# Kernel tuning notes

Hardware: AMD Instinct MI355X
Metric: run time of the kernel (lower is better)

Reference implementation:

```python
import jax, jax.numpy as jnp
import numpy as np

N_NODES = 50000
N_EDGES = 100000
NUM_RELS = 200
IN_DIM = 64
OUT_DIM = 64


def setup_inputs() -> dict:
    key = jax.random.key(0)
    k1, k2, k3, k4, k5, k6 = jax.random.split(key, 6)
    input_h = jax.random.normal(k1, (N_NODES, IN_DIM), dtype=jnp.float32)
    src = jax.random.randint(k2, (N_EDGES,), 0, N_NODES, dtype=jnp.int32)
    rel = jax.random.randint(k3, (N_EDGES,), 0, NUM_RELS, dtype=jnp.int32)
    dst = jax.random.randint(k4, (N_EDGES,), 0, N_NODES, dtype=jnp.int32)
    edges = jnp.stack([src, rel, dst], axis=1)  # (E, 3)
    # xavier_normal for relation weight: std = sqrt(2/(in+out))
    w_std = float(np.sqrt(2.0 / (IN_DIM + OUT_DIM)))
    weight = jax.random.normal(k5, (NUM_RELS, IN_DIM, OUT_DIM), dtype=jnp.float32) * w_std
    # xavier_uniform with leaky_relu(0.2) gain for self-loop weight
    gain = float(np.sqrt(2.0 / (1.0 + 0.2 ** 2)))
    bound = gain * float(np.sqrt(6.0 / (IN_DIM + OUT_DIM)))
    self_loop_weight = jax.random.uniform(
        k6, (IN_DIM, OUT_DIM), dtype=jnp.float32, minval=-bound, maxval=bound)
    return {"input_h": input_h, "edges": edges, "weight": weight,
            "self_loop_weight": self_loop_weight}


def reference(input_h, edges, weight, self_loop_weight):
    src, rel, dst = edges[:, 0], edges[:, 1], edges[:, 2]
    num_nodes = input_h.shape[0]
    num_edges = edges.shape[0]

    src_h = input_h[src]                      # (E, in) gather
    w_e = weight[rel]                         # (E, in, out) per-edge weight materialization
    msg = jnp.einsum('ei,eio->eo', src_h, w_e)  # per-edge bmm

    # torch quirk: index_matrix[dst] = arange(E) keeps the LAST write per dst,
    # so each edge's message is replaced by the message of the last edge
    # (in edge order) with the same destination.
    last_idx = jax.ops.segment_max(jnp.arange(num_edges, dtype=jnp.int32), dst,
                                   num_segments=num_nodes)  # (N,)
    msg = msg[last_idx[dst]]                  # (E, out)

    # scatter-mean aggregation by destination (nodes with no in-edges get 0)
    msg_sum = jax.ops.segment_sum(msg, dst, num_segments=num_nodes)          # (N, out)
    count = jax.ops.segment_sum(jnp.ones((num_edges,), msg.dtype), dst,
                                num_segments=num_nodes)                      # (N,)
    agg = jnp.where(count[:, None] > 0, msg_sum / jnp.maximum(count, 1.0)[:, None], 0.0)

    out = input_h @ self_loop_weight + agg    # self-loop plus aggregated messages
    return out
```

## Files before the change

kernel.cpp:

```cpp
#include <hip/hip_runtime.h>

#define N_NODES 50000
#define N_EDGES 100000
#define NUM_RELS 200
#define DIM 64
#define CAP 512
#define TILES 8
#define KPAD 72

typedef __attribute__((ext_vector_type(8))) short bf16x8;
typedef __attribute__((ext_vector_type(8))) unsigned short u16x8;
typedef __attribute__((ext_vector_type(4))) float f32x4;

#define OFF_LAST 0
#define OFF_CUR  50000
#define OFF_BN   50200
#define OFF_BS   152600
#define HB_OFF   1020032u
#define WT_OFF   7420032u

__device__ __forceinline__ unsigned short f2bf(float x) {
    union { float f; unsigned u; } v; v.f = x;
    unsigned r = v.u + 0x7FFFu + ((v.u >> 16) & 1u);
    return (unsigned short)(r >> 16);
}

#define PREP_INIT 197
#define PREP_WT   201
#define PREP_HB   782

__global__ __launch_bounds__(256) void prep_kernel(
    const float* __restrict__ h, const float* __restrict__ weight,
    const float* __restrict__ wself, int* __restrict__ ws,
    unsigned short* __restrict__ hb, unsigned short* __restrict__ wt)
{
    __shared__ float Wl[DIM * DIM];
    int b = blockIdx.x, t = threadIdx.x;

    if (b < PREP_INIT) {
        int i = b * 256 + t;
        if (i < N_NODES) ws[OFF_LAST + i] = -1;
        if (i < NUM_RELS) ws[OFF_CUR + i] = 0;
        return;
    }
    if (b < PREP_INIT + PREP_WT) {
        int rel = b - PREP_INIT;
        const float* src = (rel < NUM_RELS) ? (weight + (size_t)rel * DIM * DIM) : wself;
#pragma unroll
        for (int j = 0; j < 16; ++j) Wl[t + j * 256] = src[t + j * 256];
        __syncthreads();
        int c = t >> 2, q = t & 3;
        unsigned short tmp[16];
#pragma unroll
        for (int kk = 0; kk < 16; ++kk)
            tmp[kk] = f2bf(Wl[(q * 16 + kk) * DIM + c]);
        unsigned short* dst = wt + (size_t)rel * DIM * DIM + c * DIM + q * 16;
        *(u16x8*)dst       = *(const u16x8*)&tmp[0];
        *(u16x8*)(dst + 8) = *(const u16x8*)&tmp[8];
        return;
    }
    {
        long off = (long)(b - PREP_INIT - PREP_WT) * 4096 + (long)t * 16;
        if (off < (long)N_NODES * DIM) {
            const float4* src = (const float4*)(h + off);
            unsigned short tmp[16];
#pragma unroll
            for (int j = 0; j < 4; ++j) {
                float4 v = src[j];
                tmp[j*4+0]=f2bf(v.x); tmp[j*4+1]=f2bf(v.y);
                tmp[j*4+2]=f2bf(v.z); tmp[j*4+3]=f2bf(v.w);
            }
            *(u16x8*)(hb + off)     = *(const u16x8*)&tmp[0];
            *(u16x8*)(hb + off + 8) = *(const u16x8*)&tmp[8];
        }
    }
}

__global__ void edge_max_kernel(const int* __restrict__ edges, int* __restrict__ ws) {
    int e = blockIdx.x * 256 + threadIdx.x;
    if (e < N_EDGES) atomicMax(&ws[OFF_LAST + edges[e * 3 + 2]], e);
}

#define BUCKET_BLKS 196
#define NODE_TILES 782

__global__ __launch_bounds__(256) void bucket_self_kernel(
    const int* __restrict__ edges, const unsigned short* __restrict__ hb,
    const unsigned short* __restrict__ wt, int* __restrict__ ws,
    float* __restrict__ out)
{
    __shared__ unsigned short Wsh[DIM * KPAD];
    __shared__ unsigned short Hs[DIM * KPAD];
    int t = threadIdx.x;

    if (blockIdx.x < BUCKET_BLKS) {
        int n = blockIdx.x * 256 + t;
        if (n < N_NODES) {
            int li = ws[OFF_LAST + n];
            if (li >= 0) {
                int r = edges[li * 3 + 1];
                int s = edges[li * 3 + 0];
                int pos = atomicAdd(&ws[OFF_CUR + r], 1);
                if (pos < CAP) {
                    ws[OFF_BN + r * CAP + pos] = n;
                    ws[OFF_BS + r * CAP + pos] = s;
                }
            }
        }
        return;
    }

    int base = (blockIdx.x - BUCKET_BLKS) * 64;
    int row = t >> 2, q = t & 3;
    {
        const unsigned short* wsrc = wt + (size_t)NUM_RELS * DIM * DIM + row * DIM + q * 16;
        *(u16x8*)&Wsh[row * KPAD + q * 16]     = *(const u16x8*)wsrc;
        *(u16x8*)&Wsh[row * KPAD + q * 16 + 8] = *(const u16x8*)(wsrc + 8);
        int n = base + row; if (n >= N_NODES) n = N_NODES - 1;
        const unsigned short* hsrc = hb + (size_t)n * DIM + q * 16;
        *(u16x8*)&Hs[row * KPAD + q * 16]     = *(const u16x8*)hsrc;
        *(u16x8*)&Hs[row * KPAD + q * 16 + 8] = *(const u16x8*)(hsrc + 8);
    }
    __syncthreads();

    int l = t & 63;
    int w = __builtin_amdgcn_readfirstlane(t >> 6);
    int r16 = l & 15, kb = l >> 4;

    bf16x8 a0 = *reinterpret_cast<const bf16x8*>(&Hs[(w * 16 + r16) * KPAD + kb * 8]);
    bf16x8 a1 = *reinterpret_cast<const bf16x8*>(&Hs[(w * 16 + r16) * KPAD + 32 + kb * 8]);

    int nn[4]; bool vv[4];
#pragma unroll
    for (int r = 0; r < 4; ++r) {
        nn[r] = base + w * 16 + kb * 4 + r;
        vv[r] = nn[r] < N_NODES;
    }

#pragma unroll
    for (int n4 = 0; n4 < 4; ++n4) {
        bf16x8 b0 = *reinterpret_cast<const bf16x8*>(&Wsh[(n4 * 16 + r16) * KPAD + kb * 8]);
        bf16x8 b1 = *reinterpret_cast<const bf16x8*>(&Wsh[(n4 * 16 + r16) * KPAD + 32 + kb * 8]);
        f32x4 acc = {0.f, 0.f, 0.f, 0.f};
        acc = __builtin_amdgcn_mfma_f32_16x16x32_bf16(a0, b0, acc, 0, 0, 0);
        acc = __builtin_amdgcn_mfma_f32_16x16x32_bf16(a1, b1, acc, 0, 0, 0);
#pragma unroll
        for (int r = 0; r < 4; ++r)
            if (vv[r]) out[(size_t)nn[r] * DIM + n4 * 16 + r16] = acc[r];
    }
}

__global__ __launch_bounds__(256) void msg_kernel(
    const unsigned short* __restrict__ hb, const unsigned short* __restrict__ wt,
    const int* __restrict__ ws, float* __restrict__ out)
{
    __shared__ unsigned short Wsh[DIM * KPAD];
    __shared__ unsigned short Hs[DIM * KPAD];

    int rel = blockIdx.x >> 3;
    int tile = blockIdx.x & 7;
    int c = ws[OFF_CUR + rel];
    if (c > CAP) c = CAP;
    int start = tile * 64;
    if (start >= c) return;

    int t = threadIdx.x;
    const int* bn = ws + OFF_BN + rel * CAP;
    const int* bs = ws + OFF_BS + rel * CAP;

    int row = t >> 2, q = t & 3;
    {
        const unsigned short* wsrc = wt + (size_t)rel * DIM * DIM + row * DIM + q * 16;
        *(u16x8*)&Wsh[row * KPAD + q * 16]     = *(const u16x8*)wsrc;
        *(u16x8*)&Wsh[row * KPAD + q * 16 + 8] = *(const u16x8*)(wsrc + 8);
        int pos = start + row; if (pos >= c) pos = c - 1;
        int s = bs[pos];
        const unsigned short* hsrc = hb + (size_t)s * DIM + q * 16;
        *(u16x8*)&Hs[row * KPAD + q * 16]     = *(const u16x8*)hsrc;
        *(u16x8*)&Hs[row * KPAD + q * 16 + 8] = *(const u16x8*)(hsrc + 8);
    }
    __syncthreads();

    int l = t & 63;
    int w = __builtin_amdgcn_readfirstlane(t >> 6);
    int r16 = l & 15, kb = l >> 4;

    bf16x8 a0 = *reinterpret_cast<const bf16x8*>(&Hs[(w * 16 + r16) * KPAD + kb * 8]);
    bf16x8 a1 = *reinterpret_cast<const bf16x8*>(&Hs[(w * 16 + r16) * KPAD + 32 + kb * 8]);

    int nn[4]; bool vv[4];
#pragma unroll
    for (int r = 0; r < 4; ++r) {
        int p = start + w * 16 + kb * 4 + r;
        vv[r] = p < c;
        nn[r] = bn[vv[r] ? p : 0];
    }

#pragma unroll
    for (int n4 = 0; n4 < 4; ++n4) {
        bf16x8 b0 = *reinterpret_cast<const bf16x8*>(&Wsh[(n4 * 16 + r16) * KPAD + kb * 8]);
        bf16x8 b1 = *reinterpret_cast<const bf16x8*>(&Wsh[(n4 * 16 + r16) * KPAD + 32 + kb * 8]);
        f32x4 acc = {0.f, 0.f, 0.f, 0.f};
        acc = __builtin_amdgcn_mfma_f32_16x16x32_bf16(a0, b0, acc, 0, 0, 0);
        acc = __builtin_amdgcn_mfma_f32_16x16x32_bf16(a1, b1, acc, 0, 0, 0);
#pragma unroll
        for (int r = 0; r < 4; ++r)
            if (vv[r]) out[(size_t)nn[r] * DIM + n4 * 16 + r16] += acc[r];
    }
}

extern "C" void kernel_launch(void* const* d_in, const int* in_sizes, int n_in,
                              void* d_out, int out_size, void* d_ws, size_t ws_size,
                              hipStream_t stream) {
    const float* h      = (const float*)d_in[0];
    const int*   edges  = (const int*)d_in[1];
    const float* weight = (const float*)d_in[2];
    const float* wself  = (const float*)d_in[3];
    float* out = (float*)d_out;
    int* wsi = (int*)d_ws;
    unsigned short* hb = (unsigned short*)((char*)d_ws + HB_OFF);
    unsigned short* wt = (unsigned short*)((char*)d_ws + WT_OFF);

    prep_kernel<<<PREP_INIT + PREP_WT + PREP_HB, 256, 0, stream>>>(h, weight, wself, wsi, hb, wt);
    edge_max_kernel<<<(N_EDGES + 255) / 256, 256, 0, stream>>>(edges, wsi);
    bucket_self_kernel<<<BUCKET_BLKS + NODE_TILES, 256, 0, stream>>>(edges, hb, wt, wsi, out);
    msg_kernel<<<NUM_RELS * TILES, 256, 0, stream>>>(hb, wt, wsi, out);
}
```

Baseline: 59.78 us.

## Fuse edge-max into prep kernel, use memsets, drop LDS staging in MFMA kernels

Workspace initialisation moves to two hipMemsetAsync calls, which lets the edge atomicMax pass fold into the prep kernel and removes one kernel launch. The h-to-bf16 conversion now handles 32 elements per thread over half as many blocks. The self-loop and message kernels drop their shared-memory staging and __syncthreads and load MFMA operands straight from global memory, relying on cache for the reuse of weight tiles. The aim is less launch and barrier overhead, at the cost of redundant global loads of the weight tiles across waves and two extra memset operations.

```diff
diff --git a/kernel.cpp b/kernel.cpp
--- a/kernel.cpp
+++ b/kernel.cpp
@@ -6,7 +6,6 @@
 #define DIM 64
 #define CAP 512
 #define TILES 8
-#define KPAD 72
 
 typedef __attribute__((ext_vector_type(8))) short bf16x8;
 typedef __attribute__((ext_vector_type(8))) unsigned short u16x8;
@@ -25,63 +24,61 @@
     return (unsigned short)(r >> 16);
 }
 
-#define PREP_INIT 197
-#define PREP_WT   201
-#define PREP_HB   782
+#define K1_EDGE 391
+#define K1_WT   201
+#define K1_HC   391
 
 __global__ __launch_bounds__(256) void prep_kernel(
     const float* __restrict__ h, const float* __restrict__ weight,
-    const float* __restrict__ wself, int* __restrict__ ws,
-    unsigned short* __restrict__ hb, unsigned short* __restrict__ wt)
+    const float* __restrict__ wself, const int* __restrict__ edges,
+    int* __restrict__ ws, unsigned short* __restrict__ hb,
+    unsigned short* __restrict__ wt)
 {
     __shared__ float Wl[DIM * DIM];
     int b = blockIdx.x, t = threadIdx.x;
 
-    if (b < PREP_INIT) {
-        int i = b * 256 + t;
-        if (i < N_NODES) ws[OFF_LAST + i] = -1;
-        if (i < NUM_RELS) ws[OFF_CUR + i] = 0;
+    if (b < K1_EDGE) {
+        int e = b * 256 + t;
+        if (e < N_EDGES) atomicMax(&ws[OFF_LAST + edges[e * 3 + 2]], e);
         return;
     }
-    if (b < PREP_INIT + PREP_WT) {
-        int rel = b - PREP_INIT;
+    if (b < K1_EDGE + K1_WT) {
+        int rel = b - K1_EDGE;
         const float* src = (rel < NUM_RELS) ? (weight + (size_t)rel * DIM * DIM) : wself;
 #pragma unroll
         for (int j = 0; j < 16; ++j) Wl[t + j * 256] = src[t + j * 256];
         __syncthreads();
-        int c = t >> 2, q = t & 3;
+        int cc = t >> 2, q = t & 3;
         unsigned short tmp[16];
 #pragma unroll
         for (int kk = 0; kk < 16; ++kk)
-            tmp[kk] = f2bf(Wl[(q * 16 + kk) * DIM + c]);
-        unsigned short* dst = wt + (size_t)rel * DIM * DIM + c * DIM + q * 16;
+            tmp[kk] = f2bf(Wl[(q * 16 + kk) * DIM + cc]);
+        unsigned short* dst = wt + (size_t)rel * DIM * DIM + cc * DIM + q * 16;
         *(u16x8*)dst       = *(const u16x8*)&tmp[0];
         *(u16x8*)(dst + 8) = *(const u16x8*)&tmp[8];
         return;
     }
     {
-        long off = (long)(b - PREP_INIT - PREP_WT) * 4096 + (long)t * 16;
+        long off = (long)(b - K1_EDGE - K1_WT) * 8192 + (long)t * 32;
         if (off < (long)N_NODES * DIM) {
-            const float4* src = (const float4*)(h + off);
-            unsigned short tmp[16];
-#pragma unroll
-            for (int j = 0; j < 4; ++j) {
-                float4 v = src[j];
-                tmp[j*4+0]=f2bf(v.x); tmp[j*4+1]=f2bf(v.y);
-                tmp[j*4+2]=f2bf(v.z); tmp[j*4+3]=f2bf(v.w);
+#pragma unroll
+            for (int half = 0; half < 2; ++half) {
+                const float4* src = (const float4*)(h + off + half * 16);
+                unsigned short tmp[16];
+#pragma unroll
+                for (int j = 0; j < 4; ++j) {
+                    float4 v = src[j];
+                    tmp[j*4+0]=f2bf(v.x); tmp[j*4+1]=f2bf(v.y);
+                    tmp[j*4+2]=f2bf(v.z); tmp[j*4+3]=f2bf(v.w);
+                }
+                *(u16x8*)(hb + off + half * 16)     = *(const u16x8*)&tmp[0];
+                *(u16x8*)(hb + off + half * 16 + 8) = *(const u16x8*)&tmp[8];
             }
-            *(u16x8*)(hb + off)     = *(const u16x8*)&tmp[0];
-            *(u16x8*)(hb + off + 8) = *(const u16x8*)&tmp[8];
         }
     }
 }
 
-__global__ void edge_max_kernel(const int* __restrict__ edges, int* __restrict__ ws) {
-    int e = blockIdx.x * 256 + threadIdx.x;
-    if (e < N_EDGES) atomicMax(&ws[OFF_LAST + edges[e * 3 + 2]], e);
-}
-
-#define BUCKET_BLKS 196
+#define BK_BLKS 196
 #define NODE_TILES 782
 
 __global__ __launch_bounds__(256) void bucket_self_kernel(
@@ -89,11 +86,9 @@
     const unsigned short* __restrict__ wt, int* __restrict__ ws,
     float* __restrict__ out)
 {
-    __shared__ unsigned short Wsh[DIM * KPAD];
-    __shared__ unsigned short Hs[DIM * KPAD];
     int t = threadIdx.x;
 
-    if (blockIdx.x < BUCKET_BLKS) {
+    if (blockIdx.x < BK_BLKS) {
         int n = blockIdx.x * 256 + t;
         if (n < N_NODES) {
             int li = ws[OFF_LAST + n];
@@ -110,25 +105,18 @@
         return;
     }
 
-    int base = (blockIdx.x - BUCKET_BLKS) * 64;
-    int row = t >> 2, q = t & 3;
-    {
-        const unsigned short* wsrc = wt + (size_t)NUM_RELS * DIM * DIM + row * DIM + q * 16;
-        *(u16x8*)&Wsh[row * KPAD + q * 16]     = *(const u16x8*)wsrc;
-        *(u16x8*)&Wsh[row * KPAD + q * 16 + 8] = *(const u16x8*)(wsrc + 8);
-        int n = base + row; if (n >= N_NODES) n = N_NODES - 1;
-        const unsigned short* hsrc = hb + (size_t)n * DIM + q * 16;
-        *(u16x8*)&Hs[row * KPAD + q * 16]     = *(const u16x8*)hsrc;
-        *(u16x8*)&Hs[row * KPAD + q * 16 + 8] = *(const u16x8*)(hsrc + 8);
-    }
-    __syncthreads();
-
+    int base = (blockIdx.x - BK_BLKS) * 64;
     int l = t & 63;
     int w = __builtin_amdgcn_readfirstlane(t >> 6);
     int r16 = l & 15, kb = l >> 4;
 
-    bf16x8 a0 = *reinterpret_cast<const bf16x8*>(&Hs[(w * 16 + r16) * KPAD + kb * 8]);
-    bf16x8 a1 = *reinterpret_cast<const bf16x8*>(&Hs[(w * 16 + r16) * KPAD + 32 + kb * 8]);
+    int arow = base + w * 16 + r16;
+    if (arow >= N_NODES) arow = N_NODES - 1;
+    const unsigned short* ap = hb + (size_t)arow * DIM + kb * 8;
+    bf16x8 a0 = *reinterpret_cast<const bf16x8*>(ap);
+    bf16x8 a1 = *reinterpret_cast<const bf16x8*>(ap + 32);
+
+    const unsigned short* wts = wt + (size_t)NUM_RELS * DIM * DIM;
 
     int nn[4]; bool vv[4];
 #pragma unroll
@@ -139,8 +127,9 @@
 
 #pragma unroll
     for (int n4 = 0; n4 < 4; ++n4) {
-        bf16x8 b0 = *reinterpret_cast<const bf16x8*>(&Wsh[(n4 * 16 + r16) * KPAD + kb * 8]);
-        bf16x8 b1 = *reinterpret_cast<const bf16x8*>(&Wsh[(n4 * 16 + r16) * KPAD + 32 + kb * 8]);
+        const unsigned short* bp = wts + (n4 * 16 + r16) * DIM + kb * 8;
+        bf16x8 b0 = *reinterpret_cast<const bf16x8*>(bp);
+        bf16x8 b1 = *reinterpret_cast<const bf16x8*>(bp + 32);
         f32x4 acc = {0.f, 0.f, 0.f, 0.f};
         acc = __builtin_amdgcn_mfma_f32_16x16x32_bf16(a0, b0, acc, 0, 0, 0);
         acc = __builtin_amdgcn_mfma_f32_16x16x32_bf16(a1, b1, acc, 0, 0, 0);
@@ -154,9 +143,6 @@
     const unsigned short* __restrict__ hb, const unsigned short* __restrict__ wt,
     const int* __restrict__ ws, float* __restrict__ out)
 {
-    __shared__ unsigned short Wsh[DIM * KPAD];
-    __shared__ unsigned short Hs[DIM * KPAD];
-
     int rel = blockIdx.x >> 3;
     int tile = blockIdx.x & 7;
     int c = ws[OFF_CUR + rel];
@@ -165,28 +151,20 @@
     if (start >= c) return;
 
     int t = threadIdx.x;
-    const int* bn = ws + OFF_BN + rel * CAP;
-    const int* bs = ws + OFF_BS + rel * CAP;
-
-    int row = t >> 2, q = t & 3;
-    {
-        const unsigned short* wsrc = wt + (size_t)rel * DIM * DIM + row * DIM + q * 16;
-        *(u16x8*)&Wsh[row * KPAD + q * 16]     = *(const u16x8*)wsrc;
-        *(u16x8*)&Wsh[row * KPAD + q * 16 + 8] = *(const u16x8*)(wsrc + 8);
-        int pos = start + row; if (pos >= c) pos = c - 1;
-        int s = bs[pos];
-        const unsigned short* hsrc = hb + (size_t)s * DIM + q * 16;
-        *(u16x8*)&Hs[row * KPAD + q * 16]     = *(const u16x8*)hsrc;
-        *(u16x8*)&Hs[row * KPAD + q * 16 + 8] = *(const u16x8*)(hsrc + 8);
-    }
-    __syncthreads();
-
     int l = t & 63;
     int w = __builtin_amdgcn_readfirstlane(t >> 6);
     int r16 = l & 15, kb = l >> 4;
-
-    bf16x8 a0 = *reinterpret_cast<const bf16x8*>(&Hs[(w * 16 + r16) * KPAD + kb * 8]);
-    bf16x8 a1 = *reinterpret_cast<const bf16x8*>(&Hs[(w * 16 + r16) * KPAD + 32 + kb * 8]);
+    const int* bn = ws + OFF_BN + rel * CAP;
+    const int* bs = ws + OFF_BS + rel * CAP;
+
+    int pa = start + w * 16 + r16;
+    if (pa >= c) pa = c - 1;
+    int s = bs[pa];
+    const unsigned short* ap = hb + (size_t)s * DIM + kb * 8;
+    bf16x8 a0 = *reinterpret_cast<const bf16x8*>(ap);
+    bf16x8 a1 = *reinterpret_cast<const bf16x8*>(ap + 32);
+
+    const unsigned short* wr = wt + (size_t)rel * DIM * DIM;
 
     int nn[4]; bool vv[4];
 #pragma unroll
@@ -198,8 +176,9 @@
 
 #pragma unroll
     for (int n4 = 0; n4 < 4; ++n4) {
-        bf16x8 b0 = *reinterpret_cast<const bf16x8*>(&Wsh[(n4 * 16 + r16) * KPAD + kb * 8]);
-        bf16x8 b1 = *reinterpret_cast<const bf16x8*>(&Wsh[(n4 * 16 + r16) * KPAD + 32 + kb * 8]);
+        const unsigned short* bp = wr + (n4 * 16 + r16) * DIM + kb * 8;
+        bf16x8 b0 = *reinterpret_cast<const bf16x8*>(bp);
+        bf16x8 b1 = *reinterpret_cast<const bf16x8*>(bp + 32);
         f32x4 acc = {0.f, 0.f, 0.f, 0.f};
         acc = __builtin_amdgcn_mfma_f32_16x16x32_bf16(a0, b0, acc, 0, 0, 0);
         acc = __builtin_amdgcn_mfma_f32_16x16x32_bf16(a1, b1, acc, 0, 0, 0);
@@ -221,8 +200,10 @@
     unsigned short* hb = (unsigned short*)((char*)d_ws + HB_OFF);
     unsigned short* wt = (unsigned short*)((char*)d_ws + WT_OFF);
 
-    prep_kernel<<<PREP_INIT + PREP_WT + PREP_HB, 256, 0, stream>>>(h, weight, wself, wsi, hb, wt);
-    edge_max_kernel<<<(N_EDGES + 255) / 256, 256, 0, stream>>>(edges, wsi);
-    bucket_self_kernel<<<BUCKET_BLKS + NODE_TILES, 256, 0, stream>>>(edges, hb, wt, wsi, out);
+    hipMemsetAsync((char*)d_ws + (size_t)OFF_LAST * 4, 0xFF, (size_t)N_NODES * 4, stream);
+    hipMemsetAsync((char*)d_ws + (size_t)OFF_CUR * 4, 0, (size_t)NUM_RELS * 4, stream);
+
+    prep_kernel<<<K1_EDGE + K1_WT + K1_HC, 256, 0, stream>>>(h, weight, wself, edges, wsi, hb, wt);
+    bucket_self_kernel<<<BK_BLKS + NODE_TILES, 256, 0, stream>>>(edges, hb, wt, wsi, out);
     msg_kernel<<<NUM_RELS * TILES, 256, 0, stream>>>(hb, wt, wsi, out);
 }
```

After: 70.65 us. +18.2%, slower.

## Drop bf16 prep pass; convert fp32 tiles on the fly and memset workspace

Applied to the files above, without the earlier changes.

Removes the separate prep kernel that converted h and all relation weights to bf16 in global memory. The conversion now happens while staging into LDS inside the self-loop and message kernels. Workspace init becomes a hipMemsetAsync to 0xFF, with the per-relation counters offset by one to start from -1. The edge-max atomics move into the same launch as the self-loop GEMM. This saves a full read/write pass over h and the weights, at the cost of reading fp32 directly and doing strided transposed weight loads per block.

```diff
diff --git a/kernel.cpp b/kernel.cpp
--- a/kernel.cpp
+++ b/kernel.cpp
@@ -14,10 +14,8 @@
 
 #define OFF_LAST 0
 #define OFF_CUR  50000
-#define OFF_BN   50200
-#define OFF_BS   152600
-#define HB_OFF   1020032u
-#define WT_OFF   7420032u
+#define OFF_BN   50208
+#define OFF_BS   152608
 
 __device__ __forceinline__ unsigned short f2bf(float x) {
     union { float f; unsigned u; } v; v.f = x;
@@ -25,101 +23,56 @@
     return (unsigned short)(r >> 16);
 }
 
-#define PREP_INIT 197
-#define PREP_WT   201
-#define PREP_HB   782
-
-__global__ __launch_bounds__(256) void prep_kernel(
-    const float* __restrict__ h, const float* __restrict__ weight,
-    const float* __restrict__ wself, int* __restrict__ ws,
-    unsigned short* __restrict__ hb, unsigned short* __restrict__ wt)
-{
-    __shared__ float Wl[DIM * DIM];
-    int b = blockIdx.x, t = threadIdx.x;
-
-    if (b < PREP_INIT) {
-        int i = b * 256 + t;
-        if (i < N_NODES) ws[OFF_LAST + i] = -1;
-        if (i < NUM_RELS) ws[OFF_CUR + i] = 0;
-        return;
-    }
-    if (b < PREP_INIT + PREP_WT) {
-        int rel = b - PREP_INIT;
-        const float* src = (rel < NUM_RELS) ? (weight + (size_t)rel * DIM * DIM) : wself;
+__device__ __forceinline__ void stage_w_t(const float* __restrict__ W,
+                                          unsigned short* __restrict__ Wsh, int t) {
+    int c = t >> 2, q = t & 3;
+    unsigned short tmp[16];
 #pragma unroll
-        for (int j = 0; j < 16; ++j) Wl[t + j * 256] = src[t + j * 256];
-        __syncthreads();
-        int c = t >> 2, q = t & 3;
-        unsigned short tmp[16];
-#pragma unroll
-        for (int kk = 0; kk < 16; ++kk)
-            tmp[kk] = f2bf(Wl[(q * 16 + kk) * DIM + c]);
-        unsigned short* dst = wt + (size_t)rel * DIM * DIM + c * DIM + q * 16;
-        *(u16x8*)dst       = *(const u16x8*)&tmp[0];
-        *(u16x8*)(dst + 8) = *(const u16x8*)&tmp[8];
-        return;
-    }
-    {
-        long off = (long)(b - PREP_INIT - PREP_WT) * 4096 + (long)t * 16;
-        if (off < (long)N_NODES * DIM) {
-            const float4* src = (const float4*)(h + off);
-            unsigned short tmp[16];
-#pragma unroll
-            for (int j = 0; j < 4; ++j) {
-                float4 v = src[j];
-                tmp[j*4+0]=f2bf(v.x); tmp[j*4+1]=f2bf(v.y);
-                tmp[j*4+2]=f2bf(v.z); tmp[j*4+3]=f2bf(v.w);
-            }
-            *(u16x8*)(hb + off)     = *(const u16x8*)&tmp[0];
-            *(u16x8*)(hb + off + 8) = *(const u16x8*)&tmp[8];
-        }
-    }
+    for (int kk = 0; kk < 16; ++kk)
+        tmp[kk] = f2bf(W[(q * 16 + kk) * DIM + c]);
+    *(u16x8*)&Wsh[c * KPAD + q * 16]     = *(const u16x8*)&tmp[0];
+    *(u16x8*)&Wsh[c * KPAD + q * 16 + 8] = *(const u16x8*)&tmp[8];
 }
 
-__global__ void edge_max_kernel(const int* __restrict__ edges, int* __restrict__ ws) {
-    int e = blockIdx.x * 256 + threadIdx.x;
-    if (e < N_EDGES) atomicMax(&ws[OFF_LAST + edges[e * 3 + 2]], e);
+__device__ __forceinline__ void stage_h_row(const float* __restrict__ hrow,
+                                            unsigned short* __restrict__ Hs,
+                                            int row, int q) {
+    const float4* src = (const float4*)(hrow + q * 16);
+    unsigned short tmp[16];
+#pragma unroll
+    for (int j = 0; j < 4; ++j) {
+        float4 v = src[j];
+        tmp[j*4+0] = f2bf(v.x); tmp[j*4+1] = f2bf(v.y);
+        tmp[j*4+2] = f2bf(v.z); tmp[j*4+3] = f2bf(v.w);
+    }
+    *(u16x8*)&Hs[row * KPAD + q * 16]     = *(const u16x8*)&tmp[0];
+    *(u16x8*)&Hs[row * KPAD + q * 16 + 8] = *(const u16x8*)&tmp[8];
 }
 
-#define BUCKET_BLKS 196
+#define T_EM 391
 #define NODE_TILES 782
 
-__global__ __launch_bounds__(256) void bucket_self_kernel(
-    const int* __restrict__ edges, const unsigned short* __restrict__ hb,
-    const unsigned short* __restrict__ wt, int* __restrict__ ws,
+__global__ __launch_bounds__(256) void edge_self_kernel(
+    const float* __restrict__ h, const int* __restrict__ edges,
+    const float* __restrict__ wself, int* __restrict__ ws,
     float* __restrict__ out)
 {
     __shared__ unsigned short Wsh[DIM * KPAD];
     __shared__ unsigned short Hs[DIM * KPAD];
     int t = threadIdx.x;
 
-    if (blockIdx.x < BUCKET_BLKS) {
-        int n = blockIdx.x * 256 + t;
-        if (n < N_NODES) {
-            int li = ws[OFF_LAST + n];
-            if (li >= 0) {
-                int r = edges[li * 3 + 1];
-                int s = edges[li * 3 + 0];
-                int pos = atomicAdd(&ws[OFF_CUR + r], 1);
-                if (pos < CAP) {
-                    ws[OFF_BN + r * CAP + pos] = n;
-                    ws[OFF_BS + r * CAP + pos] = s;
-                }
-            }
-        }
+    if (blockIdx.x < T_EM) {
+        int e = blockIdx.x * 256 + t;
+        if (e < N_EDGES) atomicMax(&ws[OFF_LAST + edges[e * 3 + 2]], e);
         return;
     }
 
-    int base = (blockIdx.x - BUCKET_BLKS) * 64;
-    int row = t >> 2, q = t & 3;
+    int base = (blockIdx.x - T_EM) * 64;
     {
-        const unsigned short* wsrc = wt + (size_t)NUM_RELS * DIM * DIM + row * DIM + q * 16;
-        *(u16x8*)&Wsh[row * KPAD + q * 16]     = *(const u16x8*)wsrc;
-        *(u16x8*)&Wsh[row * KPAD + q * 16 + 8] = *(const u16x8*)(wsrc + 8);
+        stage_w_t(wself, Wsh, t);
+        int row = t >> 2, q = t & 3;
         int n = base + row; if (n >= N_NODES) n = N_NODES - 1;
-        const unsigned short* hsrc = hb + (size_t)n * DIM + q * 16;
-        *(u16x8*)&Hs[row * KPAD + q * 16]     = *(const u16x8*)hsrc;
-        *(u16x8*)&Hs[row * KPAD + q * 16 + 8] = *(const u16x8*)(hsrc + 8);
+        stage_h_row(h + (size_t)n * DIM, Hs, row, q);
     }
     __syncthreads();
 
@@ -127,39 +80,48 @@
     int w = __builtin_amdgcn_readfirstlane(t >> 6);
     int r16 = l & 15, kb = l >> 4;
 
-    bf16x8 a0 = *reinterpret_cast<const bf16x8*>(&Hs[(w * 16 + r16) * KPAD + kb * 8]);
-    bf16x8 a1 = *reinterpret_cast<const bf16x8*>(&Hs[(w * 16 + r16) * KPAD + 32 + kb * 8]);
-
-    int nn[4]; bool vv[4];
-#pragma unroll
-    for (int r = 0; r < 4; ++r) {
-        nn[r] = base + w * 16 + kb * 4 + r;
-        vv[r] = nn[r] < N_NODES;
-    }
+    bf16x8 a0 = *(const bf16x8*)&Hs[(w * 16 + r16) * KPAD + kb * 8];
+    bf16x8 a1 = *(const bf16x8*)&Hs[(w * 16 + r16) * KPAD + 32 + kb * 8];
 
 #pragma unroll
     for (int n4 = 0; n4 < 4; ++n4) {
-        bf16x8 b0 = *reinterpret_cast<const bf16x8*>(&Wsh[(n4 * 16 + r16) * KPAD + kb * 8]);
-        bf16x8 b1 = *reinterpret_cast<const bf16x8*>(&Wsh[(n4 * 16 + r16) * KPAD + 32 + kb * 8]);
+        bf16x8 b0 = *(const bf16x8*)&Wsh[(n4 * 16 + r16) * KPAD + kb * 8];
+        bf16x8 b1 = *(const bf16x8*)&Wsh[(n4 * 16 + r16) * KPAD + 32 + kb * 8];
         f32x4 acc = {0.f, 0.f, 0.f, 0.f};
         acc = __builtin_amdgcn_mfma_f32_16x16x32_bf16(a0, b0, acc, 0, 0, 0);
         acc = __builtin_amdgcn_mfma_f32_16x16x32_bf16(a1, b1, acc, 0, 0, 0);
 #pragma unroll
-        for (int r = 0; r < 4; ++r)
-            if (vv[r]) out[(size_t)nn[r] * DIM + n4 * 16 + r16] = acc[r];
+        for (int r = 0; r < 4; ++r) {
+            int nn = base + w * 16 + kb * 4 + r;
+            if (nn < N_NODES) out[(size_t)nn * DIM + n4 * 16 + r16] = acc[r];
+        }
+    }
+}
+
+__global__ __launch_bounds__(256) void bucket_kernel(const int* __restrict__ edges,
+                                                     int* __restrict__ ws) {
+    int n = blockIdx.x * 256 + threadIdx.x;
+    if (n >= N_NODES) return;
+    int li = ws[OFF_LAST + n];
+    if (li < 0) return;
+    int r = edges[li * 3 + 1];
+    int s = edges[li * 3 + 0];
+    int pos = atomicAdd(&ws[OFF_CUR + r], 1) + 1;
+    if (pos < CAP) {
+        ws[OFF_BN + r * CAP + pos] = n;
+        ws[OFF_BS + r * CAP + pos] = s;
     }
 }
 
 __global__ __launch_bounds__(256) void msg_kernel(
-    const unsigned short* __restrict__ hb, const unsigned short* __restrict__ wt,
+    const float* __restrict__ h, const float* __restrict__ weight,
     const int* __restrict__ ws, float* __restrict__ out)
 {
     __shared__ unsigned short Wsh[DIM * KPAD];
     __shared__ unsigned short Hs[DIM * KPAD];
 
-    int rel = blockIdx.x >> 3;
-    int tile = blockIdx.x & 7;
-    int c = ws[OFF_CUR + rel];
+    int rel = blockIdx.x >> 3, tile = blockIdx.x & 7;
+    int c = ws[OFF_CUR + rel] + 1;
     if (c > CAP) c = CAP;
     int start = tile * 64;
     if (start >= c) return;
@@ -168,16 +130,12 @@
     const int* bn = ws + OFF_BN + rel * CAP;
     const int* bs = ws + OFF_BS + rel * CAP;
 
-    int row = t >> 2, q = t & 3;
     {
-        const unsigned short* wsrc = wt + (size_t)rel * DIM * DIM + row * DIM + q * 16;
-        *(u16x8*)&Wsh[row * KPAD + q * 16]     = *(const u16x8*)wsrc;
-        *(u16x8*)&Wsh[row * KPAD + q * 16 + 8] = *(const u16x8*)(wsrc + 8);
+        stage_w_t(weight + (size_t)rel * DIM * DIM, Wsh, t);
+        int row = t >> 2, q = t & 3;
         int pos = start + row; if (pos >= c) pos = c - 1;
         int s = bs[pos];
-        const unsigned short* hsrc = hb + (size_t)s * DIM + q * 16;
-        *(u16x8*)&Hs[row * KPAD + q * 16]     = *(const u16x8*)hsrc;
-        *(u16x8*)&Hs[row * KPAD + q * 16 + 8] = *(const u16x8*)(hsrc + 8);
+        stage_h_row(h + (size_t)s * DIM, Hs, row, q);
     }
     __syncthreads();
 
@@ -185,8 +143,8 @@
     int w = __builtin_amdgcn_readfirstlane(t >> 6);
     int r16 = l & 15, kb = l >> 4;
 
-    bf16x8 a0 = *reinterpret_cast<const bf16x8*>(&Hs[(w * 16 + r16) * KPAD + kb * 8]);
-    bf16x8 a1 = *reinterpret_cast<const bf16x8*>(&Hs[(w * 16 + r16) * KPAD + 32 + kb * 8]);
+    bf16x8 a0 = *(const bf16x8*)&Hs[(w * 16 + r16) * KPAD + kb * 8];
+    bf16x8 a1 = *(const bf16x8*)&Hs[(w * 16 + r16) * KPAD + 32 + kb * 8];
 
     int nn[4]; bool vv[4];
 #pragma unroll
@@ -198,8 +156,8 @@
 
 #pragma unroll
     for (int n4 = 0; n4 < 4; ++n4) {
-        bf16x8 b0 = *reinterpret_cast<const bf16x8*>(&Wsh[(n4 * 16 + r16) * KPAD + kb * 8]);
-        bf16x8 b1 = *reinterpret_cast<const bf16x8*>(&Wsh[(n4 * 16 + r16) * KPAD + 32 + kb * 8]);
+        bf16x8 b0 = *(const bf16x8*)&Wsh[(n4 * 16 + r16) * KPAD + kb * 8];
+        bf16x8 b1 = *(const bf16x8*)&Wsh[(n4 * 16 + r16) * KPAD + 32 + kb * 8];
         f32x4 acc = {0.f, 0.f, 0.f, 0.f};
         acc = __builtin_amdgcn_mfma_f32_16x16x32_bf16(a0, b0, acc, 0, 0, 0);
         acc = __builtin_amdgcn_mfma_f32_16x16x32_bf16(a1, b1, acc, 0, 0, 0);
@@ -217,12 +175,11 @@
     const float* weight = (const float*)d_in[2];
     const float* wself  = (const float*)d_in[3];
     float* out = (float*)d_out;
-    int* wsi = (int*)d_ws;
-    unsigned short* hb = (unsigned short*)((char*)d_ws + HB_OFF);
-    unsigned short* wt = (unsigned short*)((char*)d_ws + WT_OFF);
+    int* ws = (int*)d_ws;
 
-    prep_kernel<<<PREP_INIT + PREP_WT + PREP_HB, 256, 0, stream>>>(h, weight, wself, wsi, hb, wt);
-    edge_max_kernel<<<(N_EDGES + 255) / 256, 256, 0, stream>>>(edges, wsi);
-    bucket_self_kernel<<<BUCKET_BLKS + NODE_TILES, 256, 0, stream>>>(edges, hb, wt, wsi, out);
-    msg_kernel<<<NUM_RELS * TILES, 256, 0, stream>>>(hb, wt, wsi, out);
+    hipMemsetAsync(d_ws, 0xFF, (size_t)(N_NODES + 208) * 4, stream);
+
+    edge_self_kernel<<<T_EM + NODE_TILES, 256, 0, stream>>>(h, edges, wself, ws, out);
+    bucket_kernel<<<(N_NODES + 255) / 256, 256, 0, stream>>>(edges, ws);
+    msg_kernel<<<NUM_RELS * TILES, 256, 0, stream>>>(h, weight, ws, out);
 }
```

After: 67.04 us. 1.12x slower.

## Fold edge-max into prep kernel and replace init blocks with memset

Applied to the files above, without the earlier changes.

Workspace initialization moves to a hipMemsetAsync that fills both last-index and per-relation counters with -1. The counters are biased by +1 at the two places they are read. The edge atomicMax pass is merged into prep_kernel as extra blocks, which removes a separate launch. This relies on ordering, because the atomicMax blocks run concurrently with the weight and bf16 conversion blocks and need the memset to finish before them. The h-to-bf16 conversion blocks now handle 32 elements per thread instead of 16, halving their block count.

```diff
diff --git a/kernel.cpp b/kernel.cpp
--- a/kernel.cpp
+++ b/kernel.cpp
@@ -14,8 +14,8 @@
 
 #define OFF_LAST 0
 #define OFF_CUR  50000
-#define OFF_BN   50200
-#define OFF_BS   152600
+#define OFF_BN   50208
+#define OFF_BS   152608
 #define HB_OFF   1020032u
 #define WT_OFF   7420032u
 
@@ -25,63 +25,61 @@
     return (unsigned short)(r >> 16);
 }
 
-#define PREP_INIT 197
-#define PREP_WT   201
-#define PREP_HB   782
+#define T_EM 391
+#define T_WT 201
+#define T_HC 391
 
 __global__ __launch_bounds__(256) void prep_kernel(
     const float* __restrict__ h, const float* __restrict__ weight,
-    const float* __restrict__ wself, int* __restrict__ ws,
-    unsigned short* __restrict__ hb, unsigned short* __restrict__ wt)
+    const float* __restrict__ wself, const int* __restrict__ edges,
+    int* __restrict__ ws, unsigned short* __restrict__ hb,
+    unsigned short* __restrict__ wt)
 {
     __shared__ float Wl[DIM * DIM];
     int b = blockIdx.x, t = threadIdx.x;
 
-    if (b < PREP_INIT) {
-        int i = b * 256 + t;
-        if (i < N_NODES) ws[OFF_LAST + i] = -1;
-        if (i < NUM_RELS) ws[OFF_CUR + i] = 0;
+    if (b < T_EM) {
+        int e = b * 256 + t;
+        if (e < N_EDGES) atomicMax(&ws[OFF_LAST + edges[e * 3 + 2]], e);
         return;
     }
-    if (b < PREP_INIT + PREP_WT) {
-        int rel = b - PREP_INIT;
+    if (b < T_EM + T_WT) {
+        int rel = b - T_EM;
         const float* src = (rel < NUM_RELS) ? (weight + (size_t)rel * DIM * DIM) : wself;
 #pragma unroll
         for (int j = 0; j < 16; ++j) Wl[t + j * 256] = src[t + j * 256];
         __syncthreads();
-        int c = t >> 2, q = t & 3;
+        int cc = t >> 2, q = t & 3;
         unsigned short tmp[16];
 #pragma unroll
         for (int kk = 0; kk < 16; ++kk)
-            tmp[kk] = f2bf(Wl[(q * 16 + kk) * DIM + c]);
-        unsigned short* dst = wt + (size_t)rel * DIM * DIM + c * DIM + q * 16;
+            tmp[kk] = f2bf(Wl[(q * 16 + kk) * DIM + cc]);
+        unsigned short* dst = wt + (size_t)rel * DIM * DIM + cc * DIM + q * 16;
         *(u16x8*)dst       = *(const u16x8*)&tmp[0];
         *(u16x8*)(dst + 8) = *(const u16x8*)&tmp[8];
         return;
     }
     {
-        long off = (long)(b - PREP_INIT - PREP_WT) * 4096 + (long)t * 16;
+        long off = (long)(b - T_EM - T_WT) * 8192 + (long)t * 32;
         if (off < (long)N_NODES * DIM) {
-            const float4* src = (const float4*)(h + off);
-            unsigned short tmp[16];
-#pragma unroll
-            for (int j = 0; j < 4; ++j) {
-                float4 v = src[j];
-                tmp[j*4+0]=f2bf(v.x); tmp[j*4+1]=f2bf(v.y);
-                tmp[j*4+2]=f2bf(v.z); tmp[j*4+3]=f2bf(v.w);
+#pragma unroll
+            for (int half = 0; half < 2; ++half) {
+                const float4* src = (const float4*)(h + off + half * 16);
+                unsigned short tmp[16];
+#pragma unroll
+                for (int j = 0; j < 4; ++j) {
+                    float4 v = src[j];
+                    tmp[j*4+0]=f2bf(v.x); tmp[j*4+1]=f2bf(v.y);
+                    tmp[j*4+2]=f2bf(v.z); tmp[j*4+3]=f2bf(v.w);
+                }
+                *(u16x8*)(hb + off + half * 16)     = *(const u16x8*)&tmp[0];
+                *(u16x8*)(hb + off + half * 16 + 8) = *(const u16x8*)&tmp[8];
             }
-            *(u16x8*)(hb + off)     = *(const u16x8*)&tmp[0];
-            *(u16x8*)(hb + off + 8) = *(const u16x8*)&tmp[8];
         }
     }
 }
 
-__global__ void edge_max_kernel(const int* __restrict__ edges, int* __restrict__ ws) {
-    int e = blockIdx.x * 256 + threadIdx.x;
-    if (e < N_EDGES) atomicMax(&ws[OFF_LAST + edges[e * 3 + 2]], e);
-}
-
-#define BUCKET_BLKS 196
+#define BK_BLKS 196
 #define NODE_TILES 782
 
 __global__ __launch_bounds__(256) void bucket_self_kernel(
@@ -93,14 +91,14 @@
     __shared__ unsigned short Hs[DIM * KPAD];
     int t = threadIdx.x;
 
-    if (blockIdx.x < BUCKET_BLKS) {
+    if (blockIdx.x < BK_BLKS) {
         int n = blockIdx.x * 256 + t;
         if (n < N_NODES) {
             int li = ws[OFF_LAST + n];
             if (li >= 0) {
                 int r = edges[li * 3 + 1];
                 int s = edges[li * 3 + 0];
-                int pos = atomicAdd(&ws[OFF_CUR + r], 1);
+                int pos = atomicAdd(&ws[OFF_CUR + r], 1) + 1;
                 if (pos < CAP) {
                     ws[OFF_BN + r * CAP + pos] = n;
                     ws[OFF_BS + r * CAP + pos] = s;
@@ -110,7 +108,7 @@
         return;
     }
 
-    int base = (blockIdx.x - BUCKET_BLKS) * 64;
+    int base = (blockIdx.x - BK_BLKS) * 64;
     int row = t >> 2, q = t & 3;
     {
         const unsigned short* wsrc = wt + (size_t)NUM_RELS * DIM * DIM + row * DIM + q * 16;
@@ -159,7 +157,7 @@
 
     int rel = blockIdx.x >> 3;
     int tile = blockIdx.x & 7;
-    int c = ws[OFF_CUR + rel];
+    int c = ws[OFF_CUR + rel] + 1;
     if (c > CAP) c = CAP;
     int start = tile * 64;
     if (start >= c) return;
@@ -221,8 +219,9 @@
     unsigned short* hb = (unsigned short*)((char*)d_ws + HB_OFF);
     unsigned short* wt = (unsigned short*)((char*)d_ws + WT_OFF);
 
-    prep_kernel<<<PREP_INIT + PREP_WT + PREP_HB, 256, 0, stream>>>(h, weight, wself, wsi, hb, wt);
-    edge_max_kernel<<<(N_EDGES + 255) / 256, 256, 0, stream>>>(edges, wsi);
-    bucket_self_kernel<<<BUCKET_BLKS + NODE_TILES, 256, 0, stream>>>(edges, hb, wt, wsi, out);
+    hipMemsetAsync(d_ws, 0xFF, (size_t)(N_NODES + 208) * 4, stream);
+
+    prep_kernel<<<T_EM + T_WT + T_HC, 256, 0, stream>>>(h, weight, wself, edges, wsi, hb, wt);
+    bucket_self_kernel<<<BK_BLKS + NODE_TILES, 256, 0, stream>>>(edges, hb, wt, wsi, out);
     msg_kernel<<<NUM_RELS * TILES, 256, 0, stream>>>(hb, wt, wsi, out);
 }
```

New measurement: 62.76 us. +5.0%, slower.
